# Kernel optimization log

Measured on AMD Instinct MI355X. Metric: run time of the kernel, lower is better.

## Reference

```python
import jax, jax.numpy as jnp
import numpy as np

B, E, C = 128, 16, 128   # batch, n experts (program tokens), module_dim
H = W = 64               # input image size
PROJ, FC, NANS = 512, 1024, 2


def conv2d(x, w, b, padding=1):
    # x: [N,C,H,W], w: [O,I,kh,kw]
    y = jax.lax.conv_general_dilated(
        x, w, (1, 1), [(padding, padding), (padding, padding)],
        dimension_numbers=('NCHW', 'OIHW', 'NCHW'))
    return y + b[None, :, None, None]


def maxpool2(x):
    return jax.lax.reduce_window(x, -jnp.inf, jax.lax.max, (1, 1, 2, 2), (1, 1, 2, 2), 'VALID')


def setup_inputs() -> dict:
    key = jax.random.key(0)
    ks = jax.random.split(key, 12)
    def init(k, shape, fan_in):
        return jax.random.normal(k, shape, jnp.float32) * np.float32(1.0 / np.sqrt(fan_in))
    inp = {}
    inp['image'] = jax.random.normal(ks[0], (B, 3, H, W), jnp.float32)
    inp['question'] = jax.random.randint(ks[1], (B, 8), 0, E)
    # stem: conv3x3 3->C, relu, maxpool2, conv3x3 C->C, relu, maxpool2
    inp['stem_w1'] = init(ks[2], (C, 3, 3, 3), 3 * 9)
    inp['stem_b1'] = jnp.zeros((C,), jnp.float32)
    inp['stem_w2'] = init(ks[3], (C, C, 3, 3), C * 9)
    inp['stem_b2'] = jnp.zeros((C,), jnp.float32)
    # E expert residual blocks, each: conv3x3 C->C, relu, conv3x3 C->C, +res, relu
    inp['exp_w1'] = init(ks[4], (E, C, C, 3, 3), C * 9)
    inp['exp_b1'] = jnp.zeros((E, C), jnp.float32)
    inp['exp_w2'] = init(ks[5], (E, C, C, 3, 3), C * 9)
    inp['exp_b2'] = jnp.zeros((E, C), jnp.float32)
    # classifier: 1x1 conv C->PROJ, relu, maxpool2, flatten, fc->FC, relu, fc->NANS
    inp['proj_w'] = init(ks[6], (PROJ, C, 1, 1), C)
    inp['proj_b'] = jnp.zeros((PROJ,), jnp.float32)
    inp['fc1_w'] = init(ks[7], (FC, PROJ * 8 * 8), PROJ * 8 * 8)
    inp['fc1_b'] = jnp.zeros((FC,), jnp.float32)
    inp['fc2_w'] = init(ks[8], (NANS, FC), FC)
    inp['fc2_b'] = jnp.zeros((NANS,), jnp.float32)
    return inp


def reference(image, question, stem_w1, stem_b1, stem_w2, stem_b2,
              exp_w1, exp_b1, exp_w2, exp_b2,
              proj_w, proj_b, fc1_w, fc1_b, fc2_w, fc2_b):
    # stem -> [B, C, 16, 16]
    h = maxpool2(jax.nn.relu(conv2d(image, stem_w1, stem_b1)))
    h = maxpool2(jax.nn.relu(conv2d(h, stem_w2, stem_b2)))

    def block(x, w1, b1, w2, b2):
        # per-sample residual block with per-sample expert weights; x: [C,h,w]
        x4 = x[None]
        out = jax.nn.relu(conv2d(x4, w1, b1))
        out = conv2d(out, w2, b2)
        return jax.nn.relu(x4 + out)[0]

    # dispatch order matches [color_lhs, lhs, color_rhs, rhs, rel] = cols 3,4,6,7,5
    for col in (3, 4, 6, 7, 5):
        idx = question[:, col]
        h = jax.vmap(block)(h, exp_w1[idx], exp_b1[idx], exp_w2[idx], exp_b2[idx])

    # classifier
    p = maxpool2(jax.nn.relu(conv2d(h, proj_w, proj_b, padding=0)))  # [B,PROJ,8,8]
    f = p.reshape(p.shape[0], -1)
    f = jax.nn.relu(f @ fc1_w.T + fc1_b)
    return f @ fc2_w.T + fc2_b
```

## Files before the change

### kernel.cpp

```cpp
#include <hip/hip_runtime.h>
#include <hip/hip_bf16.h>
#include <cstdint>
#include <cstddef>


typedef __bf16 bf16_t;
typedef __attribute__((ext_vector_type(4))) bf16_t bf16x4;
typedef __attribute__((ext_vector_type(8))) bf16_t bf16x8;
typedef __attribute__((ext_vector_type(16))) float f32x16;
typedef __attribute__((ext_vector_type(4))) float f32x4;

__global__ __launch_bounds__(256) void wconv_frag_k(
    const float* __restrict__ in, bf16_t* __restrict__ out)
{
  const int bid = blockIdx.x;
  const int dd  = bid % 9;
  const int r1  = bid / 9;
  const int ich = r1 & 1;
  const int r2  = r1 >> 1;
  const int ocg = r2 & 3;
  const int e   = r2 >> 2;

  const int t = threadIdx.x;
  const int kh = t >> 6, lane = t & 63;
  const int g = lane >> 5, cc = lane & 31;

  const float* ip = in + (size_t)(e * 128 + ocg * 32 + cc) * 1152 + dd;
  const int ic0 = ich * 64 + kh * 16 + g * 8;

  bf16_t* op = out + (size_t)e * 147456
             + ((size_t)(((ocg * 2 + ich) * 9 + dd) * 4) << 9) + t * 8;
  bf16x8 v;
#pragma unroll
  for (int j = 0; j < 8; ++j) v[j] = (bf16_t)ip[(ic0 + j) * 9];
  *(bf16x8*)op = v;
}

__global__ __launch_bounds__(128) void pconv_frag_k(
    const float* __restrict__ in, bf16_t* __restrict__ out)
{
  const int oc = blockIdx.x;
  const int og = oc >> 5, cc = oc & 31;
  const int ic = threadIdx.x;
  const int ich = ic >> 6, icl = ic & 63;
  const int kh = icl >> 4, g = (icl >> 3) & 1, j = icl & 7;
  const int off = ((((og * 2 + ich) * 4 + kh) << 9)) + ((g << 5) + cc) * 8 + j;
  out[off] = (bf16_t)in[(size_t)oc * 128 + ic];
}

__global__ __launch_bounds__(256) void stem1_nhwc_k(
    const float* __restrict__ img, const float* __restrict__ w1,
    const float* __restrict__ b1, bf16_t* __restrict__ out)
{
  const int bid = blockIdx.x;
  const int b = bid >> 4, t = bid & 15;
  const int ty0p = (t >> 2) * 8, tx0p = (t & 3) * 8;
  const int tid = threadIdx.x, lane = tid & 63;
  const int wvbase = __builtin_amdgcn_readfirstlane(tid >> 6) * 32;

  __shared__ float sImg[3][18][19];
  __shared__ char  sOut[16384];

  for (int s = tid; s < 972; s += 256) {
    const int ic = s / 324, r2 = s - ic * 324;
    const int rr = r2 / 18, cc = r2 - rr * 18;
    const int gy = 2 * ty0p - 1 + rr, gx = 2 * tx0p - 1 + cc;
    float v = 0.f;
    if (gy >= 0 && gy < 64 && gx >= 0 && gx < 64)
      v = img[(((size_t)b * 3 + ic) * 64 + gy) * 64 + gx];
    sImg[ic][rr][cc] = v;
  }
  __syncthreads();

  const int ppy = lane >> 3, ppx = lane & 7;
  float patch[3][4][4];
#pragma unroll
  for (int ic = 0; ic < 3; ++ic)
#pragma unroll
    for (int r = 0; r < 4; ++r)
#pragma unroll
      for (int c = 0; c < 4; ++c)
        patch[ic][r][c] = sImg[ic][2 * ppy + r][2 * ppx + c];

  const int swz = (lane & 15) << 3;
  char* orow = sOut + lane * 256;
#pragma unroll 2
  for (int o4 = 0; o4 < 32; o4 += 4) {
    bf16x4 qv;
#pragma unroll
    for (int j = 0; j < 4; ++j) {
      const int oc = wvbase + o4 + j;
      const float* wp = w1 + oc * 27;
      float a[2][2];
#pragma unroll
      for (int i = 0; i < 2; ++i)
#pragma unroll
        for (int jj = 0; jj < 2; ++jj) a[i][jj] = b1[oc];
#pragma unroll
      for (int ic = 0; ic < 3; ++ic)
#pragma unroll
        for (int dy = 0; dy < 3; ++dy)
#pragma unroll
          for (int dx = 0; dx < 3; ++dx) {
            const float wv = wp[ic * 9 + dy * 3 + dx];
#pragma unroll
            for (int i = 0; i < 2; ++i)
#pragma unroll
              for (int jj = 0; jj < 2; ++jj)
                a[i][jj] = fmaf(patch[ic][i + dy][jj + dx], wv, a[i][jj]);
          }
      const float mx = fmaxf(fmaxf(a[0][0], a[0][1]), fmaxf(a[1][0], a[1][1]));
      qv[j] = (bf16_t)fmaxf(mx, 0.f);
    }
    *(bf16x4*)(orow + (((wvbase + o4) * 2) ^ swz)) = qv;
  }
  __syncthreads();

#pragma unroll
  for (int it = 0; it < 4; ++it) {
    const int idx = it * 256 + tid;
    const int px = idx >> 4, ch8 = idx & 15;
    const int sw = (px & 15) << 3;
    const char* rb = sOut + px * 256;
    bf16x4 lo = *(const bf16x4*)(rb + ((ch8 * 16) ^ sw));
    bf16x4 hi = *(const bf16x4*)(rb + ((ch8 * 16 + 8) ^ sw));
    bf16x8 v;
#pragma unroll
    for (int j = 0; j < 4; ++j) { v[j] = lo[j]; v[4 + j] = hi[j]; }
    const int gpy = ty0p + (px >> 3), gpx = tx0p + (px & 7);
    *(bf16x8*)(out + ((size_t)(b * 1024 + gpy * 32 + gpx)) * 128 + ch8 * 8) = v;
  }
}

__global__ __launch_bounds__(256) void conv_stem2_k(
    const bf16_t* __restrict__ act, const bf16_t* __restrict__ wF,
    const float* __restrict__ bias, bf16_t* __restrict__ out)
{
  const int b = blockIdx.x >> 4, ph = blockIdx.x & 15;
  const int y0 = ph * 2;
  const int tid = threadIdx.x, lane = tid & 63, wv = tid >> 6;
  const int g = lane >> 5, cc = lane & 31;
  const int wq = wv;

  __shared__ bf16_t simg[272 * 64];

  f32x16 acc[2];
#pragma unroll
  for (int i = 0; i < 2; ++i)
#pragma unroll
    for (int r = 0; r < 16; ++r) acc[i][r] = 0.f;

  const bf16_t* wfb = wF + ((size_t)(wq * 2) * 9 * 4 << 9) + lane * 8;

  for (int p = tid; p < 272; p += 256) {
    const int ich = p / 136, r2 = p - ich * 136;
    const int yy = r2 / 34, xx = r2 - yy * 34;
    const int gy = y0 + yy - 1, gx = xx - 1;
    const bool inb = (gy >= 0 && gy < 32 && gx >= 0 && gx < 32);
    const bf16_t* src = act + ((size_t)(b * 1024 + gy * 32 + gx)) * 128 + ich * 64;
#pragma unroll
    for (int j = 0; j < 8; ++j) {
      bf16x8 v = {};
      if (inb) v = *(const bf16x8*)(src + j * 8);
      const int waddr = (p * 128 + j * 16) ^ ((p & 7) << 4);
      *(bf16x8*)((char*)simg + waddr) = v;
    }
  }
  __syncthreads();

#pragma unroll
  for (int ich = 0; ich < 2; ++ich) {
#pragma unroll
    for (int dydx = 0; dydx < 9; ++dydx) {
      const int dy = dydx / 3, dx = dydx - dy * 3;
      const bf16_t* wf = wfb + (((ich * 9 + dydx) * 4) << 9);
#pragma unroll
      for (int kh = 0; kh < 4; ++kh) {
        const bf16x8 a = *(const bf16x8*)(wf + (kh << 9));
#pragma unroll
        for (int r = 0; r < 2; ++r) {
          const int s = ich * 136 + (r + dy) * 34 + cc + dx;
          const int raddr = (s * 128 + (kh * 2 + g) * 16) ^ ((s & 7) << 4);
          const bf16x8 bbv = *(const bf16x8*)((const char*)simg + raddr);
          acc[r] = __builtin_amdgcn_mfma_f32_32x32x16_bf16(a, bbv, acc[r], 0, 0, 0);
        }
      }
    }
  }

  const int pxp = cc >> 1;
  bf16_t* op = out + ((size_t)(b * 256 + ph * 16 + pxp)) * 128;
#pragma unroll
  for (int rq = 0; rq < 4; ++rq) {
    const int oc4 = wq * 32 + rq * 8 + g * 4;
    const f32x4 bi = *(const f32x4*)(bias + oc4);
    bf16x4 qv;
#pragma unroll
    for (int j = 0; j < 4; ++j) {
      const int r = rq * 4 + j;
      float v = fmaxf(acc[0][r], acc[1][r]);
      v = fmaxf(v, __shfl_xor(v, 1));
      qv[j] = (bf16_t)fmaxf(v + bi[j], 0.f);
    }
    if ((cc & 1) == 0) *(bf16x4*)(op + oc4) = qv;
  }
}

template<int RES>
__global__ __launch_bounds__(256) void conv_exp_k(
    const bf16_t* __restrict__ act, const bf16_t* __restrict__ wF,
    const float* __restrict__ bias, const int* __restrict__ question, int col,
    const bf16_t* __restrict__ res, bf16_t* __restrict__ out)
{
  const int b = blockIdx.x >> 2, ph = blockIdx.x & 3;
  const int y0 = ph * 4;
  const int e = question[b * 8 + col];
  const int tid = threadIdx.x, lane = tid & 63, wv = tid >> 6;
  const int g = lane >> 5, cc = lane & 31;
  const int wq_oc = wv & 1, wq_px = wv >> 1;

  __shared__ bf16_t simg[216 * 64];

  f32x16 acc[2];
#pragma unroll
  for (int i = 0; i < 2; ++i)
#pragma unroll
    for (int r = 0; r < 16; ++r) acc[i][r] = 0.f;

  const int px = wq_px * 32 + cc;
  const int sl = (px >> 4) * 18 + (px & 15);

  const bf16_t* wfb = wF + (size_t)e * 147456
                    + (((size_t)(wq_oc * 2) * 2) * 9 * 4 << 9) + lane * 8;

  for (int p = tid; p < 216; p += 256) {
    const int ich = p / 108, r2 = p - ich * 108;
    const int yy = r2 / 18, xx = r2 - yy * 18;
    const int gy = y0 + yy - 1, gx = xx - 1;
    const bool inb = (gy >= 0 && gy < 16 && gx >= 0 && gx < 16);
    const bf16_t* src = act + ((size_t)(b * 256 + gy * 16 + gx)) * 128 + ich * 64;
#pragma unroll
    for (int j = 0; j < 8; ++j) {
      bf16x8 v = {};
      if (inb) v = *(const bf16x8*)(src + j * 8);
      const int waddr = (p * 128 + j * 16) ^ ((p & 7) << 4);
      *(bf16x8*)((char*)simg + waddr) = v;
    }
  }
  __syncthreads();

#pragma unroll
  for (int ich = 0; ich < 2; ++ich) {
#pragma unroll
    for (int dydx = 0; dydx < 9; ++dydx) {
      const int dy = dydx / 3, dx = dydx - dy * 3;
      const int sbase = ich * 108 + sl + dy * 18 + dx;
      const bf16_t* wf = wfb + (((ich * 9 + dydx) * 4) << 9);
#pragma unroll
      for (int kh = 0; kh < 4; ++kh) {
        const bf16x8 a0 = *(const bf16x8*)(wf + (kh << 9));
        const bf16x8 a1 = *(const bf16x8*)(wf + 36864 + (kh << 9));
        const int raddr = (sbase * 128 + (kh * 2 + g) * 16) ^ ((sbase & 7) << 4);
        const bf16x8 bbv = *(const bf16x8*)((const char*)simg + raddr);
        acc[0] = __builtin_amdgcn_mfma_f32_32x32x16_bf16(a0, bbv, acc[0], 0, 0, 0);
        acc[1] = __builtin_amdgcn_mfma_f32_32x32x16_bf16(a1, bbv, acc[1], 0, 0, 0);
      }
    }
  }

  const float* bb = bias + e * 128;
  const size_t pixbase = ((size_t)(b * 256 + (y0 + (px >> 4)) * 16 + (px & 15))) * 128;
  bf16_t* op = out + pixbase;
#pragma unroll
  for (int mf = 0; mf < 2; ++mf) {
#pragma unroll
    for (int rq = 0; rq < 4; ++rq) {
      const int oc4 = wq_oc * 64 + mf * 32 + rq * 8 + g * 4;
      const f32x4 bi = *(const f32x4*)(bb + oc4);
      bf16x4 qv;
      bf16x4 rv = {};
      if (RES) rv = *(const bf16x4*)(res + pixbase + oc4);
#pragma unroll
      for (int j = 0; j < 4; ++j) {
        float v = acc[mf][rq * 4 + j] + bi[j];
        if (RES) v += (float)rv[j];
        qv[j] = (bf16_t)fmaxf(v, 0.f);
      }
      *(bf16x4*)(op + oc4) = qv;
    }
  }
}

__global__ __launch_bounds__(256) void proj_mfma_k(
    const bf16_t* __restrict__ h, const bf16_t* __restrict__ pwF,
    const float* __restrict__ pb, bf16_t* __restrict__ f)
{
  const int b = blockIdx.x >> 2, ocg = blockIdx.x & 3;
  const int tid = threadIdx.x, lane = tid & 63, wv = tid >> 6;
  const int g = lane >> 5, cc = lane & 31;
  const int wq_oc = wv & 1, wq_px = wv >> 1;

  __shared__ bf16_t simg[256 * 64];

  f32x16 acc[2][4];
#pragma unroll
  for (int i = 0; i < 2; ++i)
#pragma unroll
    for (int j = 0; j < 4; ++j)
#pragma unroll
      for (int r = 0; r < 16; ++r) acc[i][j][r] = 0.f;

  const int px0 = wq_px * 128 + cc;
  const int og0 = ocg * 4 + wq_oc * 2;
  const bf16_t* pfb = pwF + (((size_t)og0 * 2 * 4) << 9) + lane * 8;

  for (int ich = 0; ich < 2; ++ich) {
    __syncthreads();
    {
      const int p = tid;
      const bf16_t* src = h + ((size_t)(b * 256 + p)) * 128 + ich * 64;
#pragma unroll
      for (int j = 0; j < 8; ++j) {
        bf16x8 v = *(const bf16x8*)(src + j * 8);
        const int waddr = (p * 128 + j * 16) ^ ((p & 7) << 4);
        *(bf16x8*)((char*)simg + waddr) = v;
      }
    }
    __syncthreads();

#pragma unroll
    for (int kh = 0; kh < 4; ++kh) {
      const bf16x8 a0 = *(const bf16x8*)(pfb + ((ich * 4 + kh) << 9));
      const bf16x8 a1 = *(const bf16x8*)(pfb + 4096 + ((ich * 4 + kh) << 9));
#pragma unroll
      for (int nf = 0; nf < 4; ++nf) {
        const int s = px0 + nf * 32;
        const int raddr = (s * 128 + (kh * 2 + g) * 16) ^ ((s & 7) << 4);
        const bf16x8 bb = *(const bf16x8*)((const char*)simg + raddr);
        acc[0][nf] = __builtin_amdgcn_mfma_f32_32x32x16_bf16(a0, bb, acc[0][nf], 0, 0, 0);
        acc[1][nf] = __builtin_amdgcn_mfma_f32_32x32x16_bf16(a1, bb, acc[1][nf], 0, 0, 0);
      }
    }
  }

#pragma unroll
  for (int mf = 0; mf < 2; ++mf) {
#pragma unroll
    for (int nf = 0; nf < 4; ++nf) {
      const int px = px0 + nf * 32;
      const int x = px & 15;
      const int py = wq_px * 4 + nf;
      const int pxp = x >> 1;
#pragma unroll
      for (int r = 0; r < 16; ++r) {
        float v = acc[mf][nf][r];
        v = fmaxf(v, __shfl_xor(v, 1));
        v = fmaxf(v, __shfl_xor(v, 16));
        const int oc = ocg * 128 + wq_oc * 64 + mf * 32 + (r & 3) + 8 * (r >> 2) + 4 * g;
        v = fmaxf(v + pb[oc], 0.f);
        if ((cc & 17) == 0)
          f[((size_t)(b * 512 + oc)) * 64 + py * 8 + pxp] = (bf16_t)v;
      }
    }
  }
}

__global__ __launch_bounds__(256) void fc1_mfma_k(
    const bf16_t* __restrict__ A, const float* __restrict__ W,
    float* __restrict__ part)
{
  const int nt = blockIdx.x;
  const int ks = blockIdx.y;
  const int n0 = nt * 64;
  const int k0 = ks * 1024;
  const int tid = threadIdx.x, lane = tid & 63, wv = tid >> 6;
  const int g = lane >> 5, cc = lane & 31;
  const int mh = wv & 1, nh = wv >> 1;

  __shared__ char sA[16384];
  __shared__ char sB[8192];

  f32x16 acc0, acc1;
#pragma unroll
  for (int r = 0; r < 16; ++r) { acc0[r] = 0.f; acc1[r] = 0.f; }

  for (int t = 0; t < 16; ++t) {
    __syncthreads();
#pragma unroll
    for (int i = 0; i < 4; ++i) {
      const int c = tid + i * 256;
      const int row = c >> 3, ko = c & 7;
      bf16x8 v = *(const bf16x8*)(A + (size_t)row * 32768 + k0 + t * 64 + ko * 8);
      const int wa = (row * 128 + ko * 16) ^ ((row & 7) << 4);
      *(bf16x8*)(sA + wa) = v;
    }
#pragma unroll
    for (int i = 0; i < 2; ++i) {
      const int c = tid + i * 256;
      const int row = c >> 3, ko = c & 7;
      const float* src = W + (size_t)(n0 + row) * 32768 + k0 + t * 64 + ko * 8;
      f32x4 u0 = *(const f32x4*)src;
      f32x4 u1 = *(const f32x4*)(src + 4);
      bf16x8 v;
#pragma unroll
      for (int j = 0; j < 4; ++j) { v[j] = (bf16_t)u0[j]; v[4 + j] = (bf16_t)u1[j]; }
      const int wa = (row * 128 + ko * 16) ^ ((row & 7) << 4);
      *(bf16x8*)(sB + wa) = v;
    }
    __syncthreads();
#pragma unroll
    for (int kss = 0; kss < 4; ++kss) {
      const int kb = kss * 32 + g * 16;
      const int rA0 = mh * 64 + cc, rA1 = rA0 + 32;
      const bf16x8 a0 = *(const bf16x8*)(sA + ((rA0 * 128 + kb) ^ ((rA0 & 7) << 4)));
      const bf16x8 a1 = *(const bf16x8*)(sA + ((rA1 * 128 + kb) ^ ((rA1 & 7) << 4)));
      const int rB = nh * 32 + cc;
      const bf16x8 bb = *(const bf16x8*)(sB + ((rB * 128 + kb) ^ ((rB & 7) << 4)));
      acc0 = __builtin_amdgcn_mfma_f32_32x32x16_bf16(a0, bb, acc0, 0, 0, 0);
      acc1 = __builtin_amdgcn_mfma_f32_32x32x16_bf16(a1, bb, acc1, 0, 0, 0);
    }
  }

  float* pp = part + ((size_t)ks * 128) * 1024 + n0 + nh * 32 + cc;
#pragma unroll
  for (int r = 0; r < 16; ++r) {
    const int m0 = mh * 64 + (r & 3) + 8 * (r >> 2) + 4 * g;
    pp[(size_t)m0 * 1024] = acc0[r];
    pp[(size_t)(m0 + 32) * 1024] = acc1[r];
  }
}

__global__ __launch_bounds__(256) void fc1_red_k(
    const float* __restrict__ part, const float* __restrict__ bias, float* __restrict__ fo)
{
  const int i = blockIdx.x * 256 + threadIdx.x;
  const int m = i >> 10, j = i & 1023;
  float s = bias[j];
#pragma unroll
  for (int ks = 0; ks < 32; ++ks) s += part[((size_t)ks * 128 + m) * 1024 + j];
  fo[i] = fmaxf(s, 0.f);
}

__global__ __launch_bounds__(256) void fc2_k(
    const float* __restrict__ fo, const float* __restrict__ w2,
    const float* __restrict__ b2, float* __restrict__ out)
{
  const int m = blockIdx.x;
  const int tid = threadIdx.x;
  float a0 = 0.f, a1 = 0.f;
  for (int k = tid; k < 1024; k += 256) {
    const float fv = fo[(size_t)m * 1024 + k];
    a0 = fmaf(fv, w2[k], a0);
    a1 = fmaf(fv, w2[1024 + k], a1);
  }
#pragma unroll
  for (int o = 32; o > 0; o >>= 1) {
    a0 += __shfl_down(a0, o);
    a1 += __shfl_down(a1, o);
  }
  __shared__ float r0[4], r1[4];
  const int wid = tid >> 6;
  if ((tid & 63) == 0) { r0[wid] = a0; r1[wid] = a1; }
  __syncthreads();
  if (tid == 0) {
    out[(size_t)m * 2 + 0] = r0[0] + r0[1] + r0[2] + r0[3] + b2[0];
    out[(size_t)m * 2 + 1] = r1[0] + r1[1] + r1[2] + r1[3] + b2[1];
  }
}

extern "C" void kernel_launch(void* const* d_in, const int* in_sizes, int n_in,
                              void* d_out, int out_size, void* d_ws, size_t ws_size,
                              hipStream_t stream)
{
  const float* image    = (const float*)d_in[0];
  const int*   question = (const int*)  d_in[1];
  const float* stem_w1  = (const float*)d_in[2];
  const float* stem_b1  = (const float*)d_in[3];
  const float* stem_w2  = (const float*)d_in[4];
  const float* stem_b2  = (const float*)d_in[5];
  const float* exp_w1   = (const float*)d_in[6];
  const float* exp_b1   = (const float*)d_in[7];
  const float* exp_w2   = (const float*)d_in[8];
  const float* exp_b2   = (const float*)d_in[9];
  const float* proj_w   = (const float*)d_in[10];
  const float* proj_b   = (const float*)d_in[11];
  const float* fc1_w    = (const float*)d_in[12];
  const float* fc1_b    = (const float*)d_in[13];
  const float* fc2_w    = (const float*)d_in[14];
  const float* fc2_b    = (const float*)d_in[15];
  float* out = (float*)d_out;

  char* base = (char*)d_ws;
  bf16_t* actA   = (bf16_t*)(base + 33554432);
  bf16_t* actH   = (bf16_t*)(base + 67108864);
  bf16_t* actT   = (bf16_t*)(base + 75497472);
  bf16_t* wT1    = (bf16_t*)(base + 83886080);
  bf16_t* wT2    = (bf16_t*)(base + 88604672);
  bf16_t* wTs2   = (bf16_t*)(base + 93323264);
  bf16_t* pwT    = (bf16_t*)(base + 93618176);
  bf16_t* fbf  = (bf16_t*)base;
  float*  part = (float*)(base + 8388608);
  float*  f1o  = (float*)(base + 25165824);

  wconv_frag_k<<<1152, 256, 0, stream>>>(exp_w1, wT1);
  wconv_frag_k<<<1152, 256, 0, stream>>>(exp_w2, wT2);
  wconv_frag_k<<<72, 256, 0, stream>>>(stem_w2, wTs2);
  pconv_frag_k<<<512, 128, 0, stream>>>(proj_w, pwT);

  stem1_nhwc_k<<<2048, 256, 0, stream>>>(image, stem_w1, stem_b1, actA);
  conv_stem2_k<<<2048, 256, 0, stream>>>(actA, wTs2, stem_b2, actH);

  const int cols[5] = {3, 4, 6, 7, 5};
  for (int i = 0; i < 5; ++i) {
    conv_exp_k<0><<<512, 256, 0, stream>>>(actH, wT1, exp_b1, question, cols[i],
                                           nullptr, actT);
    conv_exp_k<1><<<512, 256, 0, stream>>>(actT, wT2, exp_b2, question, cols[i],
                                           actH, actH);
  }

  proj_mfma_k<<<512, 256, 0, stream>>>(actH, pwT, proj_b, fbf);
  fc1_mfma_k<<<dim3(16, 32), 256, 0, stream>>>(fbf, fc1_w, part);
  fc1_red_k<<<512, 256, 0, stream>>>(part, fc1_b, f1o);
  fc2_k<<<128, 256, 0, stream>>>(f1o, fc2_w, fc2_b, out);
}
```

Before: 381.9 us.

## Widen fc1 GEMM N tile to 128 and double split-K factor

The fc1 split-K GEMM now gives each block a 128-wide N tile with a 2x2 MFMA accumulator per wave, and halves the K chunk to 512 so the grid becomes 8x64 blocks. The wider tile means each streamed A tile is reused across twice as many output columns, and the A (activation) traffic falls with fewer N tiles. In exchange the partial-sum buffer doubles to 64 slices, which adds write and read traffic in the reduction kernel, and the f1o buffer is moved to avoid overlapping it.

```diff
diff --git a/kernel.cpp b/kernel.cpp
--- a/kernel.cpp
+++ b/kernel.cpp
@@ -371,20 +371,24 @@
 {
   const int nt = blockIdx.x;
   const int ks = blockIdx.y;
-  const int n0 = nt * 64;
-  const int k0 = ks * 1024;
+  const int n0 = nt * 128;
+  const int k0 = ks * 512;
   const int tid = threadIdx.x, lane = tid & 63, wv = tid >> 6;
   const int g = lane >> 5, cc = lane & 31;
   const int mh = wv & 1, nh = wv >> 1;
 
   __shared__ char sA[16384];
-  __shared__ char sB[8192];
-
-  f32x16 acc0, acc1;
-#pragma unroll
-  for (int r = 0; r < 16; ++r) { acc0[r] = 0.f; acc1[r] = 0.f; }
-
-  for (int t = 0; t < 16; ++t) {
+  __shared__ char sB[16384];
+
+  f32x16 acc[2][2];
+#pragma unroll
+  for (int im = 0; im < 2; ++im)
+#pragma unroll
+    for (int in = 0; in < 2; ++in)
+#pragma unroll
+      for (int r = 0; r < 16; ++r) acc[im][in][r] = 0.f;
+
+  for (int t = 0; t < 8; ++t) {
     __syncthreads();
 #pragma unroll
     for (int i = 0; i < 4; ++i) {
@@ -395,7 +399,7 @@
       *(bf16x8*)(sA + wa) = v;
     }
 #pragma unroll
-    for (int i = 0; i < 2; ++i) {
+    for (int i = 0; i < 4; ++i) {
       const int c = tid + i * 256;
       const int row = c >> 3, ko = c & 7;
       const float* src = W + (size_t)(n0 + row) * 32768 + k0 + t * 64 + ko * 8;
@@ -412,22 +416,29 @@
     for (int kss = 0; kss < 4; ++kss) {
       const int kb = kss * 32 + g * 16;
       const int rA0 = mh * 64 + cc, rA1 = rA0 + 32;
+      const int rB0 = nh * 64 + cc, rB1 = rB0 + 32;
       const bf16x8 a0 = *(const bf16x8*)(sA + ((rA0 * 128 + kb) ^ ((rA0 & 7) << 4)));
       const bf16x8 a1 = *(const bf16x8*)(sA + ((rA1 * 128 + kb) ^ ((rA1 & 7) << 4)));
-      const int rB = nh * 32 + cc;
-      const bf16x8 bb = *(const bf16x8*)(sB + ((rB * 128 + kb) ^ ((rB & 7) << 4)));
-      acc0 = __builtin_amdgcn_mfma_f32_32x32x16_bf16(a0, bb, acc0, 0, 0, 0);
-      acc1 = __builtin_amdgcn_mfma_f32_32x32x16_bf16(a1, bb, acc1, 0, 0, 0);
-    }
-  }
-
-  float* pp = part + ((size_t)ks * 128) * 1024 + n0 + nh * 32 + cc;
-#pragma unroll
-  for (int r = 0; r < 16; ++r) {
-    const int m0 = mh * 64 + (r & 3) + 8 * (r >> 2) + 4 * g;
-    pp[(size_t)m0 * 1024] = acc0[r];
-    pp[(size_t)(m0 + 32) * 1024] = acc1[r];
-  }
+      const bf16x8 b0 = *(const bf16x8*)(sB + ((rB0 * 128 + kb) ^ ((rB0 & 7) << 4)));
+      const bf16x8 b1 = *(const bf16x8*)(sB + ((rB1 * 128 + kb) ^ ((rB1 & 7) << 4)));
+      acc[0][0] = __builtin_amdgcn_mfma_f32_32x32x16_bf16(a0, b0, acc[0][0], 0, 0, 0);
+      acc[0][1] = __builtin_amdgcn_mfma_f32_32x32x16_bf16(a0, b1, acc[0][1], 0, 0, 0);
+      acc[1][0] = __builtin_amdgcn_mfma_f32_32x32x16_bf16(a1, b0, acc[1][0], 0, 0, 0);
+      acc[1][1] = __builtin_amdgcn_mfma_f32_32x32x16_bf16(a1, b1, acc[1][1], 0, 0, 0);
+    }
+  }
+
+#pragma unroll
+  for (int im = 0; im < 2; ++im)
+#pragma unroll
+    for (int in = 0; in < 2; ++in) {
+      float* pp = part + ((size_t)ks * 128) * 1024 + n0 + nh * 64 + in * 32 + cc;
+#pragma unroll
+      for (int r = 0; r < 16; ++r) {
+        const int m0 = mh * 64 + im * 32 + (r & 3) + 8 * (r >> 2) + 4 * g;
+        pp[(size_t)m0 * 1024] = acc[im][in][r];
+      }
+    }
 }
 
 __global__ __launch_bounds__(256) void fc1_red_k(
@@ -436,8 +447,8 @@
   const int i = blockIdx.x * 256 + threadIdx.x;
   const int m = i >> 10, j = i & 1023;
   float s = bias[j];
-#pragma unroll
-  for (int ks = 0; ks < 32; ++ks) s += part[((size_t)ks * 128 + m) * 1024 + j];
+#pragma unroll 8
+  for (int ks = 0; ks < 64; ++ks) s += part[((size_t)ks * 128 + m) * 1024 + j];
   fo[i] = fmaxf(s, 0.f);
 }
 
@@ -500,7 +511,7 @@
   bf16_t* pwT    = (bf16_t*)(base + 93618176);
   bf16_t* fbf  = (bf16_t*)base;
   float*  part = (float*)(base + 8388608);
-  float*  f1o  = (float*)(base + 25165824);
+  float*  f1o  = (float*)(base + 41943040);
 
   wconv_frag_k<<<1152, 256, 0, stream>>>(exp_w1, wT1);
   wconv_frag_k<<<1152, 256, 0, stream>>>(exp_w2, wT2);
@@ -519,7 +530,7 @@
   }
 
   proj_mfma_k<<<512, 256, 0, stream>>>(actH, pwT, proj_b, fbf);
-  fc1_mfma_k<<<dim3(16, 32), 256, 0, stream>>>(fbf, fc1_w, part);
+  fc1_mfma_k<<<dim3(8, 64), 256, 0, stream>>>(fbf, fc1_w, part);
   fc1_red_k<<<512, 256, 0, stream>>>(part, fc1_b, f1o);
   fc2_k<<<128, 256, 0, stream>>>(f1o, fc2_w, fc2_b, out);
 }
```

Result: no change. 385.9 us (+1.0%).
